# Optimization experiments

Measured on AMD Instinct MI355X. Metric: run time of the kernel, lower is better.

Reference implementation:

```python
import jax, jax.numpy as jnp
import numpy as np

B, L, HID, LOW = 1024, 64, 512, 20
TEMP = 1.0
EPS = 1e-20


def setup_inputs() -> dict:
    key = jax.random.key(0)
    ks = jax.random.split(key, 8)
    input_h = jax.random.normal(ks[0], (B, L, HID), jnp.float32)
    input_c = jax.random.normal(ks[1], (B, L, HID), jnp.float32)
    length = jax.random.randint(ks[2], (B,), L // 2, L + 1)          # valid lengths in [L/2, L]
    u_noise = jax.random.uniform(ks[3], (L - 1, B, L - 1), jnp.float32)  # gumbel uniforms per level
    s = 1.0 / np.sqrt(HID)
    W_reduce = jax.random.uniform(ks[4], (HID, LOW), jnp.float32, -s, s)
    b_reduce = jnp.zeros((LOW,), jnp.float32)
    s2 = 1.0 / np.sqrt(2 * LOW)
    W_comp = jax.random.uniform(ks[5], (2 * LOW, 5 * LOW), jnp.float32, -s2, s2)
    b_comp = jnp.zeros((5 * LOW,), jnp.float32)
    query = jax.random.normal(ks[6], (LOW,), jnp.float32) / np.sqrt(LOW)
    return dict(input_h=input_h, input_c=input_c, W_reduce=W_reduce, b_reduce=b_reduce,
                W_comp=W_comp, b_comp=b_comp, query=query, u_noise=u_noise, length=length)


def _treelstm(hl, cl, hr, cr, W, b):
    # BinaryTreeLSTMLayer.forward: concat children, one Linear to 5 gates
    v = jnp.concatenate([hl, hr], axis=-1) @ W + b          # (B, n, 5*LOW)
    i_, fl, fr, u_, o = jnp.split(v, 5, axis=-1)
    c = cl * jax.nn.sigmoid(fl + 1.0) + cr * jax.nn.sigmoid(fr + 1.0) \
        + jnp.tanh(u_) * jax.nn.sigmoid(i_)
    h = jax.nn.sigmoid(o) * jnp.tanh(c)
    return h, c


def _masked_softmax(logits, mask):
    probs = jax.nn.softmax(logits, axis=1)
    probs = probs * mask + EPS
    return probs / probs.sum(axis=1, keepdims=True)


def _st_gumbel(logits, u, mask):
    g = -jnp.log(-jnp.log(u + EPS) + EPS)                   # gumbel noise (non-diff, matches .data)
    y = _masked_softmax((logits + g) / TEMP, mask)
    y_hard = jax.nn.one_hot(jnp.argmax(y, axis=1), y.shape[1], dtype=y.dtype)
    return jax.lax.stop_gradient(y_hard - y) + y            # straight-through


def _forward(input_h, input_c, W_reduce, b_reduce, W_comp, b_comp, query, u_noise, length):
    h = input_h @ W_reduce + b_reduce                       # (B, L, LOW)  reduce_dim
    c = input_c @ W_reduce + b_reduce
    length_mask = (jnp.arange(L)[None, :] < length[:, None]).astype(h.dtype)  # (B, L)
    for i in range(L - 1):                                  # sequential DP over pyramid levels
        hl, cl = h[:, :-1], c[:, :-1]
        hr, cr = h[:, 1:], c[:, 1:]
        nh, nc = _treelstm(hl, cl, hr, cr, W_comp, b_comp)  # (B, L-1-i, LOW) all adjacent merges
        if i < L - 2:
            logits = nh @ query                             # dot_nd scoring, (B, L-1-i)
            sel = _st_gumbel(logits, u_noise[i, :, :L - 1 - i], length_mask[:, i + 1:])
            cum = jnp.cumsum(sel, axis=1)
            left = (1.0 - cum)[..., None]                   # keep old left spans
            right = (cum - sel)[..., None]                  # shift old right spans
            se = sel[..., None]
            nh = se * nh + left * hl + right * hr
            nc = se * nc + left * cl + right * cr
        done = length_mask[:, i + 1][:, None, None]         # update_state done_mask
        h = done * nh + (1.0 - done) * hl
        c = done * nc + (1.0 - done) * cl
    return h[:, 0]                                          # (B, LOW) root hidden state


def reference(input_h, input_c, W_reduce, b_reduce, W_comp, b_comp, query, u_noise, length):
    return _forward(input_h, input_c, W_reduce, b_reduce, W_comp, b_comp, query, u_noise, length)
```

## Files before the change

### kernel.cpp

```cpp
#include <hip/hip_runtime.h>
#include <cmath>
#include <cfloat>

namespace {

constexpr int kB   = 1024;
constexpr int kL   = 64;
constexpr int kHid = 512;
constexpr int kLow = 20;
constexpr int kLM1 = 63;
constexpr int kRowElems = kL * kLow;

typedef float v2f __attribute__((ext_vector_type(2)));

__device__ __forceinline__ float fsig(float x) {
  return __builtin_amdgcn_rcpf(1.0f + __expf(-x));
}
__device__ __forceinline__ float ftanhf(float x) {
  return 1.0f - 2.0f * __builtin_amdgcn_rcpf(1.0f + __expf(2.0f * x));
}
__device__ __forceinline__ int rdl_i(int v, int l) {
  return __builtin_amdgcn_readlane(v, l);
}
__device__ __forceinline__ float rdl_f(float v, int l) {
  return __int_as_float(__builtin_amdgcn_readlane(__float_as_int(v), l));
}

#define DPPI(v, ctrl) __builtin_amdgcn_update_dpp((v), (v), (ctrl), 0xF, 0xF, false)
#define DPPF(v, ctrl) __int_as_float(DPPI(__float_as_int(v), (ctrl)))
#define DPPF0(v, ctrl)                                                        \
  __int_as_float(__builtin_amdgcn_update_dpp(0, __float_as_int(v), (ctrl),    \
                                             0xF, 0xF, true))
#define UMAX_STAGE(CTRL)                                                      \
  {                                                                           \
    const unsigned o_ = (unsigned)DPPI((int)m, CTRL);                         \
    m = (m > o_) ? m : o_;                                                    \
  }

#define PKFMA(ACC, X, W)                                                      \
  asm("v_pk_fma_f32 %0, %1, %2, %0" : "+v"(ACC) : "v"(X), "v"(W))

__global__ __launch_bounds__(256, 6)
void reduce_kernel(const float* __restrict__ Xh, const float* __restrict__ Xc,
                   const float* __restrict__ W, const float* __restrict__ bv,
                   float* __restrict__ H0, float* __restrict__ C0) {
  __shared__ float xs[5184];
  __shared__ float wsm[64 * 20];

  const int bid = blockIdx.x;
  const float* __restrict__ X = (bid < kB) ? Xh : Xc;
  float* __restrict__ O       = (bid < kB) ? H0 : C0;
  const int b = bid & (kB - 1);
  X += (size_t)b * kL * kHid;
  O += (size_t)b * kRowElems;

  const int tid  = threadIdx.x;
  const int wave = tid >> 6;
  const int lane = tid & 63;

  float acc[20];
#pragma unroll
  for (int d = 0; d < 20; ++d) acc[d] = 0.0f;

  for (int ch = 0; ch < 8; ++ch) {
    __syncthreads();
#pragma unroll
    for (int r = 0; r < 4; ++r) {
      int f   = r * 256 + tid;
      int row = f >> 4;
      int c4  = (f & 15) << 2;
      float4 v = *(const float4*)(X + row * kHid + ch * 64 + c4);
      *(float4*)(xs + row * 65 + c4) = v;
    }
#pragma unroll
    for (int r = 0; r < 5; ++r) {
      int f = r * 256 + tid;
      wsm[f] = W[ch * 1280 + f];
    }
    __syncthreads();
#pragma unroll
    for (int kk = 0; kk < 16; ++kk) {
      int k = wave * 16 + kk;
      float x = xs[lane * 65 + k];
      const float4* wp = (const float4*)(wsm + k * 20);
      float4 w0 = wp[0], w1 = wp[1], w2 = wp[2], w3 = wp[3], w4 = wp[4];
      acc[0]  = fmaf(x, w0.x, acc[0]);  acc[1]  = fmaf(x, w0.y, acc[1]);
      acc[2]  = fmaf(x, w0.z, acc[2]);  acc[3]  = fmaf(x, w0.w, acc[3]);
      acc[4]  = fmaf(x, w1.x, acc[4]);  acc[5]  = fmaf(x, w1.y, acc[5]);
      acc[6]  = fmaf(x, w1.z, acc[6]);  acc[7]  = fmaf(x, w1.w, acc[7]);
      acc[8]  = fmaf(x, w2.x, acc[8]);  acc[9]  = fmaf(x, w2.y, acc[9]);
      acc[10] = fmaf(x, w2.z, acc[10]); acc[11] = fmaf(x, w2.w, acc[11]);
      acc[12] = fmaf(x, w3.x, acc[12]); acc[13] = fmaf(x, w3.y, acc[13]);
      acc[14] = fmaf(x, w3.z, acc[14]); acc[15] = fmaf(x, w3.w, acc[15]);
      acc[16] = fmaf(x, w4.x, acc[16]); acc[17] = fmaf(x, w4.y, acc[17]);
      acc[18] = fmaf(x, w4.z, acc[18]); acc[19] = fmaf(x, w4.w, acc[19]);
    }
  }

  __syncthreads();
  float* red = xs;
#pragma unroll
  for (int d = 0; d < 20; ++d) red[wave * 1280 + lane * 20 + d] = acc[d];
  __syncthreads();
#pragma unroll
  for (int r = 0; r < 5; ++r) {
    int f = r * 256 + tid;
    float s = (red[f] + red[1280 + f]) + (red[2560 + f] + red[3840 + f]);
    O[f] = s + bv[f % 20];
  }
}

#define EVAL_UNIT(A_, B2_, PS_, DD_, HN_)                                     \
  {                                                                           \
    float ai = bcs[DD_], af = bcs[20 + DD_], ag = bcs[40 + DD_],              \
          au = bcs[60 + DD_], ao = bcs[80 + DD_];                             \
    const int xa_ = (A_)*20, xb_ = (B2_)*20, wr_ = (DD_)*44;                  \
    _Pragma("unroll")                                                         \
    for (int kq = 0; kq < 10; ++kq) {                                         \
      const float4 xq = (kq < 5)                                              \
          ? *(const float4*)(h_state + xa_ + kq * 4)                          \
          : *(const float4*)(h_state + xb_ + (kq - 5) * 4);                   \
      const float4 wi = *(const float4*)(Wt + wr_ + kq * 4);                  \
      const float4 wf = *(const float4*)(Wt + 880  + wr_ + kq * 4);           \
      const float4 wg = *(const float4*)(Wt + 1760 + wr_ + kq * 4);           \
      const float4 wu = *(const float4*)(Wt + 2640 + wr_ + kq * 4);           \
      const float4 wo = *(const float4*)(Wt + 3520 + wr_ + kq * 4);           \
      ai = fmaf(xq.x, wi.x, ai); ai = fmaf(xq.y, wi.y, ai);                   \
      ai = fmaf(xq.z, wi.z, ai); ai = fmaf(xq.w, wi.w, ai);                   \
      af = fmaf(xq.x, wf.x, af); af = fmaf(xq.y, wf.y, af);                   \
      af = fmaf(xq.z, wf.z, af); af = fmaf(xq.w, wf.w, af);                   \
      ag = fmaf(xq.x, wg.x, ag); ag = fmaf(xq.y, wg.y, ag);                   \
      ag = fmaf(xq.z, wg.z, ag); ag = fmaf(xq.w, wg.w, ag);                   \
      au = fmaf(xq.x, wu.x, au); au = fmaf(xq.y, wu.y, au);                   \
      au = fmaf(xq.z, wu.z, au); au = fmaf(xq.w, wu.w, au);                   \
      ao = fmaf(xq.x, wo.x, ao); ao = fmaf(xq.y, wo.y, ao);                   \
      ao = fmaf(xq.z, wo.z, ao); ao = fmaf(xq.w, wo.w, ao);                   \
    }                                                                         \
    const float cl_ = c_state[(A_)*20 + (DD_)],                               \
                cr_ = c_state[(B2_)*20 + (DD_)];                              \
    const float cn_ = cl_ * fsig(af + 1.0f) + cr_ * fsig(ag + 1.0f) +         \
                      ftanhf(au) * fsig(ai);                                  \
    (HN_) = fsig(ao) * ftanhf(cn_);                                           \
    nh[(PS_)*20 + (DD_)] = (HN_);                                             \
    nc[(PS_)*20 + (DD_)] = cn_;                                               \
  }

#define EVAL_KS(PXA_, PXB_, PCL_, PCR_, HN_, CN_)                             \
  {                                                                           \
    const float* xp_ = half ? (PXB_) : (PXA_);                                \
    v2f x2_[10];                                                              \
    _Pragma("unroll")                                                         \
    for (int q_ = 0; q_ < 5; ++q_) {                                          \
      const float4 t_ = *(const float4*)(xp_ + q_ * 4);                       \
      x2_[q_*2+0] = (v2f){t_.x, t_.y};                                        \
      x2_[q_*2+1] = (v2f){t_.z, t_.w};                                        \
    }                                                                         \
    v2f a0_ = (v2f){0.f,0.f}, a1_ = a0_, a2_ = a0_, a3_ = a0_, a4_ = a0_;     \
    _Pragma("unroll")                                                         \
    for (int q_ = 0; q_ < 10; ++q_) {                                         \
      PKFMA(a0_, x2_[q_], W0[q_]);                                            \
      PKFMA(a1_, x2_[q_], W1[q_]);                                            \
      PKFMA(a2_, x2_[q_], W2[q_]);                                            \
      PKFMA(a3_, x2_[q_], W3[q_]);                                            \
      PKFMA(a4_, x2_[q_], W4[q_]);                                            \
    }                                                                         \
    float si_ = a0_[0] + a0_[1], sfl_ = a1_[0] + a1_[1],                      \
          sfr_ = a2_[0] + a2_[1], su_ = a3_[0] + a3_[1],                      \
          so_ = a4_[0] + a4_[1];                                              \
    si_  += __shfl_xor(si_, 32);                                              \
    sfl_ += __shfl_xor(sfl_, 32);                                             \
    sfr_ += __shfl_xor(sfr_, 32);                                             \
    su_  += __shfl_xor(su_, 32);                                              \
    so_  += __shfl_xor(so_, 32);                                              \
    si_ += bi; sfl_ += bfl; sfr_ += bfr; su_ += bu; so_ += bo;                \
    const float cl_ = (PCL_)[ddc];                                            \
    const float cr_ = (PCR_)[ddc];                                            \
    (CN_) = cl_ * fsig(sfl_ + 1.0f) + cr_ * fsig(sfr_ + 1.0f) +               \
            ftanhf(su_) * fsig(si_);                                          \
    (HN_) = fsig(so_) * ftanhf(CN_);                                          \
  }

__global__ __launch_bounds__(64, 1)
void pyramid_kernel(const float* __restrict__ H0, const float* __restrict__ C0,
                    const float* __restrict__ Wc, const float* __restrict__ bcg,
                    const float* __restrict__ query, const float* __restrict__ U,
                    const int* __restrict__ length, float* __restrict__ out) {
  __shared__ float h_state[64 * 20];
  __shared__ float c_state[64 * 20];
  __shared__ float nh[63 * 20];
  __shared__ float nc[63 * 20];
  __shared__ float Wt[100 * 44];
  __shared__ float bcs[100];
  __shared__ float qvs[20];

  const int b    = blockIdx.x;
  const int lane = threadIdx.x;
  const int half = lane >> 5;
  const int dd   = lane & 31;
  const int ddc  = dd < 20 ? dd : 19;
  int len = length[b];
  len = len < 1 ? 1 : (len > 64 ? 64 : len);

  {
    const float4* h4 = (const float4*)(H0 + (size_t)b * kRowElems);
    const float4* c4 = (const float4*)(C0 + (size_t)b * kRowElems);
#pragma unroll
    for (int r = 0; r < 5; ++r) {
      int f = r * 64 + lane;
      ((float4*)h_state)[f] = h4[f];
      ((float4*)c_state)[f] = c4[f];
    }
  }
  for (int f = lane; f < 4000; f += 64) {
    int c = f / 40, k = f - c * 40;
    Wt[c * 44 + k] = Wc[k * 100 + c];
  }
  for (int f = lane; f < 100; f += 64) bcs[f] = bcg[f];
  if (lane < 20) qvs[lane] = query[lane];

  int   idx_r  = lane;
  int   pidx_r = lane;
  float lgt_r  = -FLT_MAX;

  const int col = lane < 62 ? lane : 62;
  const float u_row0 = U[b * kLM1 + col];
  float u_c = (kLM1 > 1) ? U[1 * (kB * kLM1) + b * kLM1 + col] : 0.0f;

#pragma unroll 1
  for (int r = 0; r < 20; ++r) {
    int uu = r * 64 + lane;
    if (uu < 1260) {
      int p = uu / 20, d2 = uu - p * 20;
      float hn_;
      EVAL_UNIT(p, p + 1, p, d2, hn_);
      (void)hn_;
    }
  }
  if (lane < 63) {
    float s = 0.0f;
#pragma unroll
    for (int q = 0; q < 5; ++q) {
      const float4 t  = *(const float4*)(nh  + lane * 20 + q * 4);
      const float4 qv = *(const float4*)(qvs + q * 4);
      s = fmaf(t.x, qv.x, s); s = fmaf(t.y, qv.y, s);
      s = fmaf(t.z, qv.z, s); s = fmaf(t.w, qv.w, s);
    }
    lgt_r = s;
  }

  v2f W0[10], W1[10], W2[10], W3[10], W4[10];
#pragma unroll
  for (int q = 0; q < 5; ++q) {
    float4 t;
    t = *(const float4*)(Wt + (0  + ddc) * 44 + half * 20 + q * 4);
    W0[q*2] = (v2f){t.x, t.y}; W0[q*2+1] = (v2f){t.z, t.w};
    t = *(const float4*)(Wt + (20 + ddc) * 44 + half * 20 + q * 4);
    W1[q*2] = (v2f){t.x, t.y}; W1[q*2+1] = (v2f){t.z, t.w};
    t = *(const float4*)(Wt + (40 + ddc) * 44 + half * 20 + q * 4);
    W2[q*2] = (v2f){t.x, t.y}; W2[q*2+1] = (v2f){t.z, t.w};
    t = *(const float4*)(Wt + (60 + ddc) * 44 + half * 20 + q * 4);
    W3[q*2] = (v2f){t.x, t.y}; W3[q*2+1] = (v2f){t.z, t.w};
    t = *(const float4*)(Wt + (80 + ddc) * 44 + half * 20 + q * 4);
    W4[q*2] = (v2f){t.x, t.y}; W4[q*2+1] = (v2f){t.z, t.w};
  }
  const float bi  = bcs[ddc],      bfl = bcs[20 + ddc], bfr = bcs[40 + ddc],
              bu  = bcs[60 + ddc], bo  = bcs[80 + ddc];
  const float qq  = qvs[ddc];

  float gcur = -__logf(-__logf(u_row0 + 1e-20f) + 1e-20f);

  const int nIter = len - 1;
#pragma unroll 1
  for (int i = 0; i < nIter; ++i) {
    const int n = kL - i;

    const float zf = lgt_r + gcur;
    const unsigned ub  = __float_as_uint(zf);
    unsigned key = ((int)ub < 0) ? ~ub : (ub | 0x80000000u);
    const bool valid = (lane <= n - 2) && ((i + 1 + lane) < len);
    if (!valid) key = 0u;
    unsigned m = key;
    UMAX_STAGE(0xB1);
    UMAX_STAGE(0x4E);
    UMAX_STAGE(0x141);
    UMAX_STAGE(0x140);
    UMAX_STAGE(0x142);
    UMAX_STAGE(0x143);
    const unsigned gmax = (unsigned)rdl_i((int)m, 63);
    const unsigned long long bal = __ballot(valid && (key == gmax));
    const int k = (int)(__ffsll(bal) - 1);

    float u_d = 0.0f;
    if (i + 2 <= kLM1 - 1) u_d = U[(i + 2) * (kB * kLM1) + b * kLM1 + col];

    const int km1 = (k >= 1) ? k - 1 : 0;
    const int kp2 = (k <= n - 3) ? k + 2 : 0;
    const int tgt = rdl_i(idx_r,  k);
    const int psk = rdl_i(pidx_r, k);
    const int iA  = rdl_i(idx_r,  km1);
    const int pA  = rdl_i(pidx_r, km1);
    const int iB  = rdl_i(idx_r,  kp2);

    if (lane < 20) {
      h_state[tgt * 20 + lane] = nh[psk * 20 + lane];
      c_state[tgt * 20 + lane] = nc[psk * 20 + lane];
    }

    {
      int   sI = DPPI(idx_r,  0x101);
      int   sP = DPPI(pidx_r, 0x101);
      float sL = DPPF(lgt_r,  0x101);
      const int   bi16 = rdl_i(idx_r, 16),  bi32 = rdl_i(idx_r, 32),
                  bi48 = rdl_i(idx_r, 48);
      const int   bp16 = rdl_i(pidx_r, 16), bp32 = rdl_i(pidx_r, 32),
                  bp48 = rdl_i(pidx_r, 48);
      const float bl16 = rdl_f(lgt_r, 16),  bl32 = rdl_f(lgt_r, 32),
                  bl48 = rdl_f(lgt_r, 48);
      if (lane == 15) { sI = bi16; sP = bp16; sL = bl16; }
      if (lane == 31) { sI = bi32; sP = bp32; sL = bl32; }
      if (lane == 47) { sI = bi48; sP = bp48; sL = bl48; }
      const bool doI = (lane >= k + 1) && (lane <= n - 2);
      const bool doP = (lane >= k + 1) && (lane <= n - 3);
      if (doI) idx_r = sI;
      if (doP) { pidx_r = sP; lgt_r = sL; }
    }

    if (i < len - 2) {
      const bool hasA = (k >= 1);
      const bool hasB = (k <= n - 3);
      float hnA, cnA, hnB, cnB;
      EVAL_KS(h_state + iA * 20, nh + psk * 20,
              c_state + iA * 20, nc + psk * 20, hnA, cnA);
      EVAL_KS(nh + psk * 20, h_state + iB * 20,
              nc + psk * 20, c_state + iB * 20, hnB, cnB);
      if (hasA && half == 0 && dd < 20) {
        nh[pA * 20 + dd] = hnA;  nc[pA * 20 + dd] = cnA;
      }
      if (hasB && half == 1 && dd < 20) {
        nh[psk * 20 + dd] = hnB; nc[psk * 20 + dd] = cnB;
      }
      float pr = 0.0f;
      if (dd < 20) pr = half ? hnB * qq : hnA * qq;
      pr += DPPF0(pr, 0xB1);
      pr += DPPF0(pr, 0x4E);
      pr += DPPF0(pr, 0x141);
      pr += DPPF0(pr, 0x140);
      pr += DPPF0(pr, 0x142);
      const float vA = rdl_f(pr, 31);
      const float vB = rdl_f(pr, 63);
      if (hasA && lane == k - 1) lgt_r = vA;
      if (hasB && lane == k)     lgt_r = vB;
    }

    gcur = -__logf(-__logf(u_c + 1e-20f) + 1e-20f);
    u_c  = u_d;
  }

  const int root = rdl_i(idx_r, 0);
  if (lane < 20) {
    out[b * 20 + lane] = h_state[root * 20 + lane];
  }
}

}

extern "C" void kernel_launch(void* const* d_in, const int* in_sizes, int n_in,
                              void* d_out, int out_size, void* d_ws, size_t ws_size,
                              hipStream_t stream) {
  const float* input_h  = (const float*)d_in[0];
  const float* input_c  = (const float*)d_in[1];
  const float* W_reduce = (const float*)d_in[2];
  const float* b_reduce = (const float*)d_in[3];
  const float* W_comp   = (const float*)d_in[4];
  const float* b_comp   = (const float*)d_in[5];
  const float* query    = (const float*)d_in[6];
  const float* u_noise  = (const float*)d_in[7];
  const int*   length   = (const int*)d_in[8];
  float* out = (float*)d_out;

  float* H0 = (float*)d_ws;
  float* C0 = H0 + (size_t)kB * kL * kLow;

  reduce_kernel<<<dim3(2 * kB), dim3(256), 0, stream>>>(
      input_h, input_c, W_reduce, b_reduce, H0, C0);
  pyramid_kernel<<<dim3(kB), dim3(64), 0, stream>>>(
      H0, C0, W_comp, b_comp, query, u_noise, length, out);
}
```

Before: 171.5 us.

## Split pyramid merges across two waves and precompute gumbel noise in LDS

New measurement: 181.9 us. 1.06x slower.

```diff
diff --git a/kernel.cpp b/kernel.cpp
--- a/kernel.cpp
+++ b/kernel.cpp
@@ -109,41 +109,6 @@
     O[f] = s + bv[f % 20];
   }
 }
-
-#define EVAL_UNIT(A_, B2_, PS_, DD_, HN_)                                     \
-  {                                                                           \
-    float ai = bcs[DD_], af = bcs[20 + DD_], ag = bcs[40 + DD_],              \
-          au = bcs[60 + DD_], ao = bcs[80 + DD_];                             \
-    const int xa_ = (A_)*20, xb_ = (B2_)*20, wr_ = (DD_)*44;                  \
-    _Pragma("unroll")                                                         \
-    for (int kq = 0; kq < 10; ++kq) {                                         \
-      const float4 xq = (kq < 5)                                              \
-          ? *(const float4*)(h_state + xa_ + kq * 4)                          \
-          : *(const float4*)(h_state + xb_ + (kq - 5) * 4);                   \
-      const float4 wi = *(const float4*)(Wt + wr_ + kq * 4);                  \
-      const float4 wf = *(const float4*)(Wt + 880  + wr_ + kq * 4);           \
-      const float4 wg = *(const float4*)(Wt + 1760 + wr_ + kq * 4);           \
-      const float4 wu = *(const float4*)(Wt + 2640 + wr_ + kq * 4);           \
-      const float4 wo = *(const float4*)(Wt + 3520 + wr_ + kq * 4);           \
-      ai = fmaf(xq.x, wi.x, ai); ai = fmaf(xq.y, wi.y, ai);                   \
-      ai = fmaf(xq.z, wi.z, ai); ai = fmaf(xq.w, wi.w, ai);                   \
-      af = fmaf(xq.x, wf.x, af); af = fmaf(xq.y, wf.y, af);                   \
-      af = fmaf(xq.z, wf.z, af); af = fmaf(xq.w, wf.w, af);                   \
-      ag = fmaf(xq.x, wg.x, ag); ag = fmaf(xq.y, wg.y, ag);                   \
-      ag = fmaf(xq.z, wg.z, ag); ag = fmaf(xq.w, wg.w, ag);                   \
-      au = fmaf(xq.x, wu.x, au); au = fmaf(xq.y, wu.y, au);                   \
-      au = fmaf(xq.z, wu.z, au); au = fmaf(xq.w, wu.w, au);                   \
-      ao = fmaf(xq.x, wo.x, ao); ao = fmaf(xq.y, wo.y, ao);                   \
-      ao = fmaf(xq.z, wo.z, ao); ao = fmaf(xq.w, wo.w, ao);                   \
-    }                                                                         \
-    const float cl_ = c_state[(A_)*20 + (DD_)],                               \
-                cr_ = c_state[(B2_)*20 + (DD_)];                              \
-    const float cn_ = cl_ * fsig(af + 1.0f) + cr_ * fsig(ag + 1.0f) +         \
-                      ftanhf(au) * fsig(ai);                                  \
-    (HN_) = fsig(ao) * ftanhf(cn_);                                           \
-    nh[(PS_)*20 + (DD_)] = (HN_);                                             \
-    nc[(PS_)*20 + (DD_)] = cn_;                                               \
-  }
 
 #define EVAL_KS(PXA_, PXB_, PCL_, PCR_, HN_, CN_)                             \
   {                                                                           \
@@ -180,7 +145,16 @@
     (HN_) = fsig(so_) * ftanhf(CN_);                                          \
   }
 
-__global__ __launch_bounds__(64, 1)
+#define LOGIT_REDUCE(PR_)                                                     \
+  {                                                                           \
+    PR_ += DPPF0(PR_, 0xB1);                                                  \
+    PR_ += DPPF0(PR_, 0x4E);                                                  \
+    PR_ += DPPF0(PR_, 0x141);                                                 \
+    PR_ += DPPF0(PR_, 0x140);                                                 \
+    PR_ += DPPF0(PR_, 0x142);                                                 \
+  }
+
+__global__ __launch_bounds__(128, 2)
 void pyramid_kernel(const float* __restrict__ H0, const float* __restrict__ C0,
                     const float* __restrict__ Wc, const float* __restrict__ bcg,
                     const float* __restrict__ query, const float* __restrict__ U,
@@ -189,12 +163,14 @@
   __shared__ float c_state[64 * 20];
   __shared__ float nh[63 * 20];
   __shared__ float nc[63 * 20];
-  __shared__ float Wt[100 * 44];
-  __shared__ float bcs[100];
-  __shared__ float qvs[20];
+  __shared__ float g_lds[63 * 64];
+  __shared__ float lgt_tmp[64];
+  __shared__ float vab[2];
 
   const int b    = blockIdx.x;
-  const int lane = threadIdx.x;
+  const int tid  = threadIdx.x;
+  const int wid  = tid >> 6;
+  const int lane = tid & 63;
   const int half = lane >> 5;
   const int dd   = lane & 31;
   const int ddc  = dd < 20 ? dd : 19;
@@ -205,77 +181,78 @@
     const float4* h4 = (const float4*)(H0 + (size_t)b * kRowElems);
     const float4* c4 = (const float4*)(C0 + (size_t)b * kRowElems);
 #pragma unroll
-    for (int r = 0; r < 5; ++r) {
-      int f = r * 64 + lane;
-      ((float4*)h_state)[f] = h4[f];
-      ((float4*)c_state)[f] = c4[f];
-    }
-  }
-  for (int f = lane; f < 4000; f += 64) {
-    int c = f / 40, k = f - c * 40;
-    Wt[c * 44 + k] = Wc[k * 100 + c];
-  }
-  for (int f = lane; f < 100; f += 64) bcs[f] = bcg[f];
-  if (lane < 20) qvs[lane] = query[lane];
+    for (int r = 0; r < 3; ++r) {
+      int f = r * 128 + tid;
+      if (f < 320) {
+        ((float4*)h_state)[f] = h4[f];
+        ((float4*)c_state)[f] = c4[f];
+      }
+    }
+  }
+
+#pragma unroll 1
+  for (int f = tid; f < 63 * 64; f += 128) {
+    const int i = f >> 6, j = f & 63;
+    float g = 0.0f;
+    if (j < 63) {
+      const float u = U[(size_t)i * (kB * kLM1) + b * kLM1 + j];
+      g = -__logf(-__logf(u + 1e-20f) + 1e-20f);
+    }
+    g_lds[f] = g;
+  }
+
+  v2f W0[10], W1[10], W2[10], W3[10], W4[10];
+#pragma unroll
+  for (int j = 0; j < 10; ++j) {
+    const float* r0 = Wc + (half * 20 + 2 * j) * 100 + ddc;
+    const float* r1 = r0 + 100;
+    W0[j] = (v2f){r0[0],  r1[0]};
+    W1[j] = (v2f){r0[20], r1[20]};
+    W2[j] = (v2f){r0[40], r1[40]};
+    W3[j] = (v2f){r0[60], r1[60]};
+    W4[j] = (v2f){r0[80], r1[80]};
+  }
+  const float bi  = bcg[ddc],      bfl = bcg[20 + ddc], bfr = bcg[40 + ddc],
+              bu  = bcg[60 + ddc], bo  = bcg[80 + ddc];
+  const float qq  = query[ddc];
 
   int   idx_r  = lane;
   int   pidx_r = lane;
   float lgt_r  = -FLT_MAX;
 
-  const int col = lane < 62 ? lane : 62;
-  const float u_row0 = U[b * kLM1 + col];
-  float u_c = (kLM1 > 1) ? U[1 * (kB * kLM1) + b * kLM1 + col] : 0.0f;
+  __syncthreads();
 
 #pragma unroll 1
-  for (int r = 0; r < 20; ++r) {
-    int uu = r * 64 + lane;
-    if (uu < 1260) {
-      int p = uu / 20, d2 = uu - p * 20;
-      float hn_;
-      EVAL_UNIT(p, p + 1, p, d2, hn_);
-      (void)hn_;
-    }
-  }
-  if (lane < 63) {
-    float s = 0.0f;
-#pragma unroll
-    for (int q = 0; q < 5; ++q) {
-      const float4 t  = *(const float4*)(nh  + lane * 20 + q * 4);
-      const float4 qv = *(const float4*)(qvs + q * 4);
-      s = fmaf(t.x, qv.x, s); s = fmaf(t.y, qv.y, s);
-      s = fmaf(t.z, qv.z, s); s = fmaf(t.w, qv.w, s);
-    }
-    lgt_r = s;
-  }
-
-  v2f W0[10], W1[10], W2[10], W3[10], W4[10];
-#pragma unroll
-  for (int q = 0; q < 5; ++q) {
-    float4 t;
-    t = *(const float4*)(Wt + (0  + ddc) * 44 + half * 20 + q * 4);
-    W0[q*2] = (v2f){t.x, t.y}; W0[q*2+1] = (v2f){t.z, t.w};
-    t = *(const float4*)(Wt + (20 + ddc) * 44 + half * 20 + q * 4);
-    W1[q*2] = (v2f){t.x, t.y}; W1[q*2+1] = (v2f){t.z, t.w};
-    t = *(const float4*)(Wt + (40 + ddc) * 44 + half * 20 + q * 4);
-    W2[q*2] = (v2f){t.x, t.y}; W2[q*2+1] = (v2f){t.z, t.w};
-    t = *(const float4*)(Wt + (60 + ddc) * 44 + half * 20 + q * 4);
-    W3[q*2] = (v2f){t.x, t.y}; W3[q*2+1] = (v2f){t.z, t.w};
-    t = *(const float4*)(Wt + (80 + ddc) * 44 + half * 20 + q * 4);
-    W4[q*2] = (v2f){t.x, t.y}; W4[q*2+1] = (v2f){t.z, t.w};
-  }
-  const float bi  = bcs[ddc],      bfl = bcs[20 + ddc], bfr = bcs[40 + ddc],
-              bu  = bcs[60 + ddc], bo  = bcs[80 + ddc];
-  const float qq  = qvs[ddc];
-
-  float gcur = -__logf(-__logf(u_row0 + 1e-20f) + 1e-20f);
+  for (int p = 0; p < 16; ++p) {
+    const int pa = p * 4 + wid * 2;
+#pragma unroll
+    for (int e = 0; e < 2; ++e) {
+      const int pp = pa + e;
+      if (pp < 63) {
+        float hn, cn;
+        EVAL_KS(h_state + pp * 20, h_state + (pp + 1) * 20,
+                c_state + pp * 20, c_state + (pp + 1) * 20, hn, cn);
+        if (half == 0 && dd < 20) {
+          nh[pp * 20 + dd] = hn;  nc[pp * 20 + dd] = cn;
+        }
+        float pr = (dd < 20) ? hn * qq : 0.0f;
+        LOGIT_REDUCE(pr);
+        const float v = rdl_f(pr, 31);
+        if (lane == 0) lgt_tmp[pp] = v;
+      }
+    }
+  }
+  __syncthreads();
+  if (lane < 63) lgt_r = lgt_tmp[lane];
 
   const int nIter = len - 1;
 #pragma unroll 1
   for (int i = 0; i < nIter; ++i) {
     const int n = kL - i;
 
-    const float zf = lgt_r + gcur;
-    const unsigned ub  = __float_as_uint(zf);
+    const float g  = g_lds[(i << 6) + lane];
+    const float zf = lgt_r + g;
+    const unsigned ub = __float_as_uint(zf);
     unsigned key = ((int)ub < 0) ? ~ub : (ub | 0x80000000u);
     const bool valid = (lane <= n - 2) && ((i + 1 + lane) < len);
     if (!valid) key = 0u;
@@ -290,9 +267,6 @@
     const unsigned long long bal = __ballot(valid && (key == gmax));
     const int k = (int)(__ffsll(bal) - 1);
 
-    float u_d = 0.0f;
-    if (i + 2 <= kLM1 - 1) u_d = U[(i + 2) * (kB * kLM1) + b * kLM1 + col];
-
     const int km1 = (k >= 1) ? k - 1 : 0;
     const int kp2 = (k <= n - 3) ? k + 2 : 0;
     const int tgt = rdl_i(idx_r,  k);
@@ -301,7 +275,7 @@
     const int pA  = rdl_i(pidx_r, km1);
     const int iB  = rdl_i(idx_r,  kp2);
 
-    if (lane < 20) {
+    if (wid == 0 && lane < 20) {
       h_state[tgt * 20 + lane] = nh[psk * 20 + lane];
       c_state[tgt * 20 + lane] = nc[psk * 20 + lane];
     }
@@ -328,37 +302,42 @@
     if (i < len - 2) {
       const bool hasA = (k >= 1);
       const bool hasB = (k <= n - 3);
-      float hnA, cnA, hnB, cnB;
-      EVAL_KS(h_state + iA * 20, nh + psk * 20,
-              c_state + iA * 20, nc + psk * 20, hnA, cnA);
-      EVAL_KS(nh + psk * 20, h_state + iB * 20,
-              nc + psk * 20, c_state + iB * 20, hnB, cnB);
-      if (hasA && half == 0 && dd < 20) {
-        nh[pA * 20 + dd] = hnA;  nc[pA * 20 + dd] = cnA;
+      const float *pxa, *pxb, *pcl, *pcr;
+      int slot;
+      bool mine;
+      if (wid == 0) {
+        pxa = h_state + iA * 20;  pxb = h_state + tgt * 20;
+        pcl = c_state + iA * 20;  pcr = c_state + tgt * 20;
+        slot = pA;  mine = hasA;
+      } else {
+        pxa = nh + psk * 20;      pxb = h_state + iB * 20;
+        pcl = nc + psk * 20;      pcr = c_state + iB * 20;
+        slot = psk; mine = hasB;
       }
-      if (hasB && half == 1 && dd < 20) {
-        nh[psk * 20 + dd] = hnB; nc[psk * 20 + dd] = cnB;
+      float hn, cn;
+      EVAL_KS(pxa, pxb, pcl, pcr, hn, cn);
+      float pr = (dd < 20) ? hn * qq : 0.0f;
+      LOGIT_REDUCE(pr);
+      const float v = rdl_f(pr, 31);
+
+      __syncthreads();
+      if (mine && half == 0 && dd < 20) {
+        nh[slot * 20 + dd] = hn;  nc[slot * 20 + dd] = cn;
       }
-      float pr = 0.0f;
-      if (dd < 20) pr = half ? hnB * qq : hnA * qq;
-      pr += DPPF0(pr, 0xB1);
-      pr += DPPF0(pr, 0x4E);
-      pr += DPPF0(pr, 0x141);
-      pr += DPPF0(pr, 0x140);
-      pr += DPPF0(pr, 0x142);
-      const float vA = rdl_f(pr, 31);
-      const float vB = rdl_f(pr, 63);
+      if (lane == 0) vab[wid] = v;
+      __syncthreads();
+
+      const float vA = vab[0], vB = vab[1];
       if (hasA && lane == k - 1) lgt_r = vA;
       if (hasB && lane == k)     lgt_r = vB;
     }
-
-    gcur = -__logf(-__logf(u_c + 1e-20f) + 1e-20f);
-    u_c  = u_d;
-  }
-
-  const int root = rdl_i(idx_r, 0);
-  if (lane < 20) {
-    out[b * 20 + lane] = h_state[root * 20 + lane];
+  }
+
+  if (wid == 0) {
+    const int root = rdl_i(idx_r, 0);
+    if (lane < 20) {
+      out[b * 20 + lane] = h_state[root * 20 + lane];
+    }
   }
 }
 
@@ -383,6 +362,6 @@
 
   reduce_kernel<<<dim3(2 * kB), dim3(256), 0, stream>>>(
       input_h, input_c, W_reduce, b_reduce, H0, C0);
-  pyramid_kernel<<<dim3(kB), dim3(64), 0, stream>>>(
+  pyramid_kernel<<<dim3(kB), dim3(128), 0, stream>>>(
       H0, C0, W_comp, b_comp, query, u_noise, length, out);
 }
```

## Repartition per-step TreeLSTM gate matvec across lanes by output column pairs

Applied to the files above, without the earlier changes.

Result: faster. 159.1 us (-7.2%).

```diff
diff --git a/kernel.cpp b/kernel.cpp
--- a/kernel.cpp
+++ b/kernel.cpp
@@ -39,6 +39,15 @@
 
 #define PKFMA(ACC, X, W)                                                      \
   asm("v_pk_fma_f32 %0, %1, %2, %0" : "+v"(ACC) : "v"(X), "v"(W))
+
+#define LOGIT_REDUCE(PR_)                                                     \
+  {                                                                           \
+    PR_ += DPPF0(PR_, 0xB1);                                                  \
+    PR_ += DPPF0(PR_, 0x4E);                                                  \
+    PR_ += DPPF0(PR_, 0x141);                                                 \
+    PR_ += DPPF0(PR_, 0x140);                                                 \
+    PR_ += DPPF0(PR_, 0x142);                                                 \
+  }
 
 __global__ __launch_bounds__(256, 6)
 void reduce_kernel(const float* __restrict__ Xh, const float* __restrict__ Xc,
@@ -145,41 +154,6 @@
     nc[(PS_)*20 + (DD_)] = cn_;                                               \
   }
 
-#define EVAL_KS(PXA_, PXB_, PCL_, PCR_, HN_, CN_)                             \
-  {                                                                           \
-    const float* xp_ = half ? (PXB_) : (PXA_);                                \
-    v2f x2_[10];                                                              \
-    _Pragma("unroll")                                                         \
-    for (int q_ = 0; q_ < 5; ++q_) {                                          \
-      const float4 t_ = *(const float4*)(xp_ + q_ * 4);                       \
-      x2_[q_*2+0] = (v2f){t_.x, t_.y};                                        \
-      x2_[q_*2+1] = (v2f){t_.z, t_.w};                                        \
-    }                                                                         \
-    v2f a0_ = (v2f){0.f,0.f}, a1_ = a0_, a2_ = a0_, a3_ = a0_, a4_ = a0_;     \
-    _Pragma("unroll")                                                         \
-    for (int q_ = 0; q_ < 10; ++q_) {                                         \
-      PKFMA(a0_, x2_[q_], W0[q_]);                                            \
-      PKFMA(a1_, x2_[q_], W1[q_]);                                            \
-      PKFMA(a2_, x2_[q_], W2[q_]);                                            \
-      PKFMA(a3_, x2_[q_], W3[q_]);                                            \
-      PKFMA(a4_, x2_[q_], W4[q_]);                                            \
-    }                                                                         \
-    float si_ = a0_[0] + a0_[1], sfl_ = a1_[0] + a1_[1],                      \
-          sfr_ = a2_[0] + a2_[1], su_ = a3_[0] + a3_[1],                      \
-          so_ = a4_[0] + a4_[1];                                              \
-    si_  += __shfl_xor(si_, 32);                                              \
-    sfl_ += __shfl_xor(sfl_, 32);                                             \
-    sfr_ += __shfl_xor(sfr_, 32);                                             \
-    su_  += __shfl_xor(su_, 32);                                              \
-    so_  += __shfl_xor(so_, 32);                                              \
-    si_ += bi; sfl_ += bfl; sfr_ += bfr; su_ += bu; so_ += bo;                \
-    const float cl_ = (PCL_)[ddc];                                            \
-    const float cr_ = (PCR_)[ddc];                                            \
-    (CN_) = cl_ * fsig(sfl_ + 1.0f) + cr_ * fsig(sfr_ + 1.0f) +               \
-            ftanhf(su_) * fsig(si_);                                          \
-    (HN_) = fsig(so_) * ftanhf(CN_);                                          \
-  }
-
 __global__ __launch_bounds__(64, 1)
 void pyramid_kernel(const float* __restrict__ H0, const float* __restrict__ C0,
                     const float* __restrict__ Wc, const float* __restrict__ bcg,
@@ -192,10 +166,11 @@
   __shared__ float Wt[100 * 44];
   __shared__ float bcs[100];
   __shared__ float qvs[20];
+  __shared__ float sc[200];
 
   const int b    = blockIdx.x;
   const int lane = threadIdx.x;
-  const int half = lane >> 5;
+  const int p    = lane >> 5;
   const int dd   = lane & 31;
   const int ddc  = dd < 20 ? dd : 19;
   int len = length[b];
@@ -218,6 +193,18 @@
   for (int f = lane; f < 100; f += 64) bcs[f] = bcg[f];
   if (lane < 20) qvs[lane] = query[lane];
 
+  const bool cact = lane < 50;
+  const int  c0   = cact ? 2 * lane : 0;
+  const int  c1   = c0 + 1;
+  v2f Wv0[20], Wv1[20];
+#pragma unroll
+  for (int k2 = 0; k2 < 20; ++k2) {
+    Wv0[k2] = (v2f){Wc[(2 * k2) * 100 + c0], Wc[(2 * k2 + 1) * 100 + c0]};
+    Wv1[k2] = (v2f){Wc[(2 * k2) * 100 + c1], Wc[(2 * k2 + 1) * 100 + c1]};
+  }
+  const float bb0 = bcg[c0], bb1 = bcg[c1];
+  const float qv_r = query[ddc];
+
   int   idx_r  = lane;
   int   pidx_r = lane;
   float lgt_r  = -FLT_MAX;
@@ -230,9 +217,9 @@
   for (int r = 0; r < 20; ++r) {
     int uu = r * 64 + lane;
     if (uu < 1260) {
-      int p = uu / 20, d2 = uu - p * 20;
+      int pp = uu / 20, d2 = uu - pp * 20;
       float hn_;
-      EVAL_UNIT(p, p + 1, p, d2, hn_);
+      EVAL_UNIT(pp, pp + 1, pp, d2, hn_);
       (void)hn_;
     }
   }
@@ -248,25 +235,6 @@
     lgt_r = s;
   }
 
-  v2f W0[10], W1[10], W2[10], W3[10], W4[10];
-#pragma unroll
-  for (int q = 0; q < 5; ++q) {
-    float4 t;
-    t = *(const float4*)(Wt + (0  + ddc) * 44 + half * 20 + q * 4);
-    W0[q*2] = (v2f){t.x, t.y}; W0[q*2+1] = (v2f){t.z, t.w};
-    t = *(const float4*)(Wt + (20 + ddc) * 44 + half * 20 + q * 4);
-    W1[q*2] = (v2f){t.x, t.y}; W1[q*2+1] = (v2f){t.z, t.w};
-    t = *(const float4*)(Wt + (40 + ddc) * 44 + half * 20 + q * 4);
-    W2[q*2] = (v2f){t.x, t.y}; W2[q*2+1] = (v2f){t.z, t.w};
-    t = *(const float4*)(Wt + (60 + ddc) * 44 + half * 20 + q * 4);
-    W3[q*2] = (v2f){t.x, t.y}; W3[q*2+1] = (v2f){t.z, t.w};
-    t = *(const float4*)(Wt + (80 + ddc) * 44 + half * 20 + q * 4);
-    W4[q*2] = (v2f){t.x, t.y}; W4[q*2+1] = (v2f){t.z, t.w};
-  }
-  const float bi  = bcs[ddc],      bfl = bcs[20 + ddc], bfr = bcs[40 + ddc],
-              bu  = bcs[60 + ddc], bo  = bcs[80 + ddc];
-  const float qq  = qvs[ddc];
-
   float gcur = -__logf(-__logf(u_row0 + 1e-20f) + 1e-20f);
 
   const int nIter = len - 1;
@@ -275,7 +243,7 @@
     const int n = kL - i;
 
     const float zf = lgt_r + gcur;
-    const unsigned ub  = __float_as_uint(zf);
+    const unsigned ub = __float_as_uint(zf);
     unsigned key = ((int)ub < 0) ? ~ub : (ub | 0x80000000u);
     const bool valid = (lane <= n - 2) && ((i + 1 + lane) < len);
     if (!valid) key = 0u;
@@ -328,24 +296,58 @@
     if (i < len - 2) {
       const bool hasA = (k >= 1);
       const bool hasB = (k <= n - 3);
-      float hnA, cnA, hnB, cnB;
-      EVAL_KS(h_state + iA * 20, nh + psk * 20,
-              c_state + iA * 20, nc + psk * 20, hnA, cnA);
-      EVAL_KS(nh + psk * 20, h_state + iB * 20,
-              nc + psk * 20, c_state + iB * 20, hnB, cnB);
-      if (hasA && half == 0 && dd < 20) {
-        nh[pA * 20 + dd] = hnA;  nc[pA * 20 + dd] = cnA;
-      }
-      if (hasB && half == 1 && dd < 20) {
-        nh[psk * 20 + dd] = hnB; nc[psk * 20 + dd] = cnB;
-      }
-      float pr = 0.0f;
-      if (dd < 20) pr = half ? hnB * qq : hnA * qq;
-      pr += DPPF0(pr, 0xB1);
-      pr += DPPF0(pr, 0x4E);
-      pr += DPPF0(pr, 0x141);
-      pr += DPPF0(pr, 0x140);
-      pr += DPPF0(pr, 0x142);
+
+      v2f hA2[10], hT2[10], hB2[10];
+#pragma unroll
+      for (int q = 0; q < 5; ++q) {
+        const float4 tA = *(const float4*)(h_state + iA * 20 + q * 4);
+        const float4 tT = *(const float4*)(nh + psk * 20 + q * 4);
+        const float4 tB = *(const float4*)(h_state + iB * 20 + q * 4);
+        hA2[2*q]   = (v2f){tA.x, tA.y};  hA2[2*q+1] = (v2f){tA.z, tA.w};
+        hT2[2*q]   = (v2f){tT.x, tT.y};  hT2[2*q+1] = (v2f){tT.z, tT.w};
+        hB2[2*q]   = (v2f){tB.x, tB.y};  hB2[2*q+1] = (v2f){tB.z, tB.w};
+      }
+
+      v2f aA0 = (v2f){0.f, 0.f}, aA1 = aA0, aB0 = aA0, aB1 = aA0;
+#pragma unroll
+      for (int k2 = 0; k2 < 10; ++k2) {
+        PKFMA(aA0, hA2[k2], Wv0[k2]);
+        PKFMA(aA1, hA2[k2], Wv1[k2]);
+        PKFMA(aB0, hT2[k2], Wv0[k2]);
+        PKFMA(aB1, hT2[k2], Wv1[k2]);
+      }
+#pragma unroll
+      for (int k2 = 10; k2 < 20; ++k2) {
+        PKFMA(aA0, hT2[k2 - 10], Wv0[k2]);
+        PKFMA(aA1, hT2[k2 - 10], Wv1[k2]);
+        PKFMA(aB0, hB2[k2 - 10], Wv0[k2]);
+        PKFMA(aB1, hB2[k2 - 10], Wv1[k2]);
+      }
+
+      if (cact) {
+        *(v2f*)(sc + c0)       = (v2f){aA0[0] + aA0[1] + bb0,
+                                       aA1[0] + aA1[1] + bb1};
+        *(v2f*)(sc + 100 + c0) = (v2f){aB0[0] + aB0[1] + bb0,
+                                       aB1[0] + aB1[1] + bb1};
+      }
+
+      const float* scp = sc + p * 100;
+      const float i_ = scp[ddc],      fl_ = scp[20 + ddc],
+                  fr_ = scp[40 + ddc], u_ = scp[60 + ddc],
+                  o_ = scp[80 + ddc];
+      const float cl_ = (p == 0) ? c_state[iA * 20 + ddc] : nc[psk * 20 + ddc];
+      const float cr_ = (p == 0) ? nc[psk * 20 + ddc] : c_state[iB * 20 + ddc];
+      const float cn_ = cl_ * fsig(fl_ + 1.0f) + cr_ * fsig(fr_ + 1.0f) +
+                        ftanhf(u_) * fsig(i_);
+      const float hn_ = fsig(o_) * ftanhf(cn_);
+      const int   slot = (p == 0) ? pA : psk;
+      const bool  mine = (p == 0) ? hasA : hasB;
+      if (mine && dd < 20) {
+        nh[slot * 20 + dd] = hn_;
+        nc[slot * 20 + dd] = cn_;
+      }
+      float pr = (dd < 20) ? hn_ * qv_r : 0.0f;
+      LOGIT_REDUCE(pr);
       const float vA = rdl_f(pr, 31);
       const float vB = rdl_f(pr, 63);
       if (hasA && lane == k - 1) lgt_r = vA;
```
